# Kernel tuning notes

Measured on AMD Instinct MI355X. Metric: run time of the kernel, lower is better.

Reference implementation:

```python
import jax, jax.numpy as jnp
import numpy as np

NEG_INF = -9.0e15
ALPHA = 0.2  # leakyrelu slope


def setup_inputs() -> dict:
    key = jax.random.key(0)
    k1, k2, k3, k4, k5 = jax.random.split(key, 5)
    B, N, D_IN, D_OUT = 8, 2048, 128, 128
    h = jax.random.normal(k1, (B, N, D_IN), dtype=jnp.float32)
    adj = jax.random.randint(k2, (N, N), 0, 2, dtype=jnp.int32)
    W = jax.random.normal(k3, (D_IN, D_OUT), dtype=jnp.float32) * (1.0 / np.sqrt(D_IN))
    a_src = jax.random.normal(k4, (D_OUT,), dtype=jnp.float32) * (1.0 / np.sqrt(D_OUT))
    a_dst = jax.random.normal(k5, (D_OUT,), dtype=jnp.float32) * (1.0 / np.sqrt(D_OUT))
    return {"h": h, "adj": adj, "W": W, "a_src": a_src, "a_dst": a_dst}


def reference(h, adj, W, a_src, a_dst):
    # Wh: [B, N, D_out]
    Wh = jnp.einsum("bnd,de->bne", h, W)
    e_src = jnp.einsum("bne,e->bn", Wh, a_src)  # [B, N]
    e_dst = jnp.einsum("bne,e->bn", Wh, a_dst)  # [B, N]
    # additive attention logits: e[b,i,j] = e_src[b,i] + e_dst[b,j]
    e = e_src[:, :, None] + e_dst[:, None, :]  # [B, N, N]
    e = jnp.where(e > 0, e, ALPHA * e)  # leaky relu
    e = jnp.where(adj[None, :, :] > 0, e, NEG_INF)
    attention = jax.nn.softmax(e, axis=-1)  # [B, N, N]
    h_prime = jnp.einsum("bij,bje->bie", attention, Wh)
    return h_prime
```

## Files before the change

kernel.cpp:

```cpp
#include <hip/hip_runtime.h>
#include <stdint.h>

#define ALPHA 0.2f
#define LOG2E 1.4426950408889634f

typedef unsigned short u16;
typedef short s16x8 __attribute__((ext_vector_type(8)));
typedef float f32x4 __attribute__((ext_vector_type(4)));

union BF8 { s16x8 v; uint32_t u[4]; u16 s[8]; uint4 q; };

static __device__ __forceinline__ float bf2f(u16 u) {
  union { uint32_t i; float f; } c; c.i = ((uint32_t)u) << 16; return c.f;
}
static __device__ __forceinline__ uint32_t pk2bf(float lo, float hi) {
  uint32_t ul = __float_as_uint(lo) + 0x8000u;
  uint32_t uh = __float_as_uint(hi) + 0x8000u;
  return (ul >> 16) | (uh & 0xffff0000u);
}

static __device__ __forceinline__ void gl2lds16(const void* g, void* l) {
  __builtin_amdgcn_global_load_lds(
      (const __attribute__((address_space(1))) uint32_t*)g,
      (__attribute__((address_space(3))) uint32_t*)l, 16, 0, 0);
}

__global__ __launch_bounds__(256) void k_zero(uint32_t* __restrict__ out, int n32) {
  int gid = blockIdx.x * 256 + threadIdx.x;
  if (gid < n32) out[gid] = 0u;
}

__global__ __launch_bounds__(256) void k_pack_adj(const int* __restrict__ adj,
                                                  uint32_t* __restrict__ bits,
                                                  const u16* __restrict__ h,
                                                  int* __restrict__ flag) {
  int tid = threadIdx.x;
  int base = blockIdx.x * 256 + tid;
#pragma unroll
  for (int it = 0; it < 8; ++it) {
    int gid = base + it * (2048 * 256);
    unsigned long long m = __ballot(adj[gid] != 0);
    if ((tid & 63) == 0)
      *(unsigned long long*)(&bits[gid >> 5]) = m;
  }
  if (blockIdx.x == 0 && tid < 64) {
    u16 v = h[2 * tid];
    int e = (v >> 7) & 0xff;
    unsigned long long dm = __ballot(e >= 100 && e <= 140);
    if (tid == 0) flag[0] = (__popcll(dm) >= 48) ? 1 : 0;
  }
}

__global__ __launch_bounds__(256) void k_wh(
    const void* __restrict__ hV, const void* __restrict__ WgV,
    const void* __restrict__ aSrcV, const void* __restrict__ aDstV,
    const int* __restrict__ flag,
    u16* __restrict__ WhT, float* __restrict__ eS, float* __restrict__ eD) {
  __shared__ __align__(16) char smemRaw[34816];
  u16*   WT   = (u16*)smemRaw;
  float* tile = (float*)smemRaw;
  __shared__ float aS[128], aD[128];

  const int tid = threadIdx.x;
  const int mb = blockIdx.x * 64;
  const int isBf = *flag;

  if (isBf) {
    const u16* Wg = (const u16*)WgV;
    for (int it = 0; it < 8; ++it) {
      int idx = tid + it * 256;
      int k = idx >> 4, c0 = (idx & 15) * 8;
      uint4 w4 = *(const uint4*)(Wg + (k << 7) + c0);
      u16* wsv = (u16*)&w4;
#pragma unroll
      for (int e = 0; e < 8; ++e) WT[(c0 + e) * 136 + k] = wsv[e];
    }
    if (tid < 128) aS[tid] = bf2f(((const u16*)aSrcV)[tid]);
    else           aD[tid - 128] = bf2f(((const u16*)aDstV)[tid - 128]);
  } else {
    const float* Wg = (const float*)WgV;
    for (int it = 0; it < 8; ++it) {
      int idx = tid + it * 256;
      int k = idx >> 4, c0 = (idx & 15) * 8;
      float4 w0 = *(const float4*)(Wg + (k << 7) + c0);
      float4 w1 = *(const float4*)(Wg + (k << 7) + c0 + 4);
      float wf[8] = {w0.x, w0.y, w0.z, w0.w, w1.x, w1.y, w1.z, w1.w};
#pragma unroll
      for (int e = 0; e < 8; ++e)
        WT[(c0 + e) * 136 + k] = (u16)((__float_as_uint(wf[e]) + 0x8000u) >> 16);
    }
    if (tid < 128) aS[tid] = ((const float*)aSrcV)[tid];
    else           aD[tid - 128] = ((const float*)aDstV)[tid - 128];
  }
  __syncthreads();

  const int wv = tid >> 6, lane = tid & 63, ln = lane & 15, quad = lane >> 4;
  const int row = mb + wv * 16 + ln;

  f32x4 acc[8];
#pragma unroll
  for (int t = 0; t < 8; ++t) acc[t] = (f32x4){0.f, 0.f, 0.f, 0.f};

  if (isBf) {
    const u16* h = (const u16*)hV;
#pragma unroll
    for (int ks = 0; ks < 4; ++ks) {
      s16x8 af = *(const s16x8*)(h + (row << 7) + ks * 32 + quad * 8);
#pragma unroll
      for (int t = 0; t < 8; ++t) {
        s16x8 bfg = *(const s16x8*)(&WT[(t * 16 + ln) * 136 + ks * 32 + quad * 8]);
        acc[t] = __builtin_amdgcn_mfma_f32_16x16x32_bf16(af, bfg, acc[t], 0, 0, 0);
      }
    }
  } else {
    const float* h = (const float*)hV;
#pragma unroll
    for (int ks = 0; ks < 4; ++ks) {
      float4 a0 = *(const float4*)(h + (row << 7) + ks * 32 + quad * 8);
      float4 a1 = *(const float4*)(h + (row << 7) + ks * 32 + quad * 8 + 4);
      BF8 af;
      af.u[0] = pk2bf(a0.x, a0.y);
      af.u[1] = pk2bf(a0.z, a0.w);
      af.u[2] = pk2bf(a1.x, a1.y);
      af.u[3] = pk2bf(a1.z, a1.w);
#pragma unroll
      for (int t = 0; t < 8; ++t) {
        s16x8 bfg = *(const s16x8*)(&WT[(t * 16 + ln) * 136 + ks * 32 + quad * 8]);
        acc[t] = __builtin_amdgcn_mfma_f32_16x16x32_bf16(af.v, bfg, acc[t], 0, 0, 0);
      }
    }
  }
  __syncthreads();

#pragma unroll
  for (int t = 0; t < 8; ++t)
#pragma unroll
    for (int r = 0; r < 4; ++r)
      tile[(wv * 16 + quad * 4 + r) * 130 + t * 16 + ln] = acc[t][r];
  __syncthreads();

  if (tid < 128) {
    int r = tid & 63, grp = tid >> 6;
    const float* a = grp ? aD : aS;
    float sum = 0.f;
#pragma unroll 4
    for (int d = 0; d < 128; ++d) sum += tile[r * 130 + d] * a[d];
    int m = mb + r, b = m >> 11, n = m & 2047;
    (grp ? eD : eS)[(b << 11) + n] = sum * LOG2E;
  }

  {
    int d = tid >> 1, half = tid & 1;
    int n0 = mb & 2047, b = mb >> 11;
    uint32_t pk[16];
#pragma unroll
    for (int qq = 0; qq < 16; ++qq) {
      float v0 = tile[(half * 32 + 2 * qq) * 130 + d];
      float v1 = tile[(half * 32 + 2 * qq + 1) * 130 + d];
      pk[qq] = pk2bf(v0, v1);
    }
    uint4* dst = (uint4*)(WhT + (size_t)((b << 7) + d) * 2048 + n0 + half * 32);
#pragma unroll
    for (int c = 0; c < 4; ++c)
      dst[c] = make_uint4(pk[c * 4], pk[c * 4 + 1], pk[c * 4 + 2], pk[c * 4 + 3]);
  }
}

__global__ __launch_bounds__(512, 4) void k_attn(
    const u16* __restrict__ WhT, const float* __restrict__ eSrc,
    const float* __restrict__ eDst, const uint32_t* __restrict__ adjBits,
    const int* __restrict__ flag, void* __restrict__ outV) {
  __shared__ __align__(16) u16 bufB[2][8192];
  __shared__ __align__(16) u16 bufP[2][2048];

  const int tid = threadIdx.x;
  const int bid = (blockIdx.x & 7) * 64 + (blockIdx.x >> 3);
  const int b = bid >> 6, ig = bid & 63;
  const int i0 = ig * 32;

  const int w = tid >> 6, l = tid & 63;
  const int ln = l & 15, quad = l >> 4;
  const int s = w & 1, dh = w >> 1;

  const int gsrc = (l & 7) ^ ((l >> 3) & 7);
  const u16* whtB = WhT + ((size_t)b << 18);
  const u16* srcB = whtB + (size_t)(w * 8 + (l >> 3)) * 2048 + gsrc * 8;

  const int prow = tid >> 4, hg = tid & 15;
  const float sSp = eSrc[(b << 11) + i0 + prow];
  const float* eDb = eDst + (b << 11) + hg * 4;
  const uint32_t* adjB = adjBits + (size_t)(i0 + prow) * 64 + (hg >> 3);
  const int pOff = prow * 128 + ((hg ^ ((prow & 7) << 1)) * 8);

  int aOff[2], bOff[2][2];
#pragma unroll
  for (int jk = 0; jk < 2; ++jk) {
    aOff[jk] = (s * 16 + ln) * 128 + (((jk * 4 + quad) ^ (ln & 7)) * 16);
#pragma unroll
    for (int tt = 0; tt < 2; ++tt)
      bOff[tt][jk] = (dh * 32 + tt * 16 + ln) * 128
                   + (((jk * 4 + quad) ^ (ln & 7)) * 16);
  }

  f32x4 acc[2], accD;
  acc[0] = (f32x4){0.f, 0.f, 0.f, 0.f};
  acc[1] = (f32x4){0.f, 0.f, 0.f, 0.f};
  accD   = (f32x4){0.f, 0.f, 0.f, 0.f};

  BF8 ones;
  ones.u[0] = 0x3f803f80u; ones.u[1] = 0x3f803f80u;
  ones.u[2] = 0x3f803f80u; ones.u[3] = 0x3f803f80u;

  u16 *bBc = bufB[0], *bBn = bufB[1];
  u16 *bPc = bufP[0], *bPn = bufP[1];

  gl2lds16(srcB, bBc + w * 512);
  gl2lds16(srcB + 131072, bBc + 4096 + w * 512);
  {
    f32x4 dv = *(const f32x4*)(eDb);
    uint32_t aw = adjB[0];
    uint32_t nib = (aw >> ((hg & 7) * 4)) & 0xfu;
    float x0 = sSp + dv[0], x1 = sSp + dv[1], x2 = sSp + dv[2], x3 = sSp + dv[3];
    float p0 = exp2f(__builtin_amdgcn_fmed3f(x0, ALPHA * x0, 80.f));
    float p1 = exp2f(__builtin_amdgcn_fmed3f(x1, ALPHA * x1, 80.f));
    float p2 = exp2f(__builtin_amdgcn_fmed3f(x2, ALPHA * x2, 80.f));
    float p3 = exp2f(__builtin_amdgcn_fmed3f(x3, ALPHA * x3, 80.f));
    uint32_t m01 = ((nib & 1u) ? 0x0000ffffu : 0u) | ((nib & 2u) ? 0xffff0000u : 0u);
    uint32_t m23 = ((nib & 4u) ? 0x0000ffffu : 0u) | ((nib & 8u) ? 0xffff0000u : 0u);
    *(uint2*)((char*)bPc + pOff) = make_uint2(pk2bf(p0, p1) & m01,
                                              pk2bf(p2, p3) & m23);
  }
  __syncthreads();

  for (int t = 0; t < 32; ++t) {
    if (t + 1 < 32) {
      gl2lds16(srcB + (size_t)(t + 1) * 64, bBn + w * 512);
      gl2lds16(srcB + (size_t)(t + 1) * 64 + 131072, bBn + 4096 + w * 512);
      f32x4 dv = *(const f32x4*)(eDb + (t + 1) * 64);
      uint32_t aw = adjB[(t + 1) * 2];
      uint32_t nib = (aw >> ((hg & 7) * 4)) & 0xfu;
      float x0 = sSp + dv[0], x1 = sSp + dv[1], x2 = sSp + dv[2], x3 = sSp + dv[3];
      float p0 = exp2f(__builtin_amdgcn_fmed3f(x0, ALPHA * x0, 80.f));
      float p1 = exp2f(__builtin_amdgcn_fmed3f(x1, ALPHA * x1, 80.f));
      float p2 = exp2f(__builtin_amdgcn_fmed3f(x2, ALPHA * x2, 80.f));
      float p3 = exp2f(__builtin_amdgcn_fmed3f(x3, ALPHA * x3, 80.f));
      uint32_t m01 = ((nib & 1u) ? 0x0000ffffu : 0u) | ((nib & 2u) ? 0xffff0000u : 0u);
      uint32_t m23 = ((nib & 4u) ? 0x0000ffffu : 0u) | ((nib & 8u) ? 0xffff0000u : 0u);
      *(uint2*)((char*)bPn + pOff) = make_uint2(pk2bf(p0, p1) & m01,
                                                pk2bf(p2, p3) & m23);
    }

    s16x8 af0 = *(const s16x8*)((const char*)bPc + aOff[0]);
    s16x8 af1 = *(const s16x8*)((const char*)bPc + aOff[1]);
    s16x8 b00 = *(const s16x8*)((const char*)bBc + bOff[0][0]);
    s16x8 b10 = *(const s16x8*)((const char*)bBc + bOff[1][0]);
    s16x8 b01 = *(const s16x8*)((const char*)bBc + bOff[0][1]);
    s16x8 b11 = *(const s16x8*)((const char*)bBc + bOff[1][1]);

    __builtin_amdgcn_s_setprio(1);
    acc[0] = __builtin_amdgcn_mfma_f32_16x16x32_bf16(af0, b00, acc[0], 0, 0, 0);
    acc[1] = __builtin_amdgcn_mfma_f32_16x16x32_bf16(af0, b10, acc[1], 0, 0, 0);
    acc[0] = __builtin_amdgcn_mfma_f32_16x16x32_bf16(af1, b01, acc[0], 0, 0, 0);
    acc[1] = __builtin_amdgcn_mfma_f32_16x16x32_bf16(af1, b11, acc[1], 0, 0, 0);
    if (dh == 0) {
      accD = __builtin_amdgcn_mfma_f32_16x16x32_bf16(af0, ones.v, accD, 0, 0, 0);
      accD = __builtin_amdgcn_mfma_f32_16x16x32_bf16(af1, ones.v, accD, 0, 0, 0);
    }
    __builtin_amdgcn_s_setprio(0);

    __syncthreads();
    u16* tB = bBc; bBc = bBn; bBn = tB;
    u16* tP = bPc; bPc = bPn; bPn = tP;
  }

  float* den = (float*)bufP;
  if (dh == 0 && ln == 0) {
#pragma unroll
    for (int r = 0; r < 4; ++r) den[s * 16 + quad * 4 + r] = accD[r];
  }
  __syncthreads();

  float inv[4];
#pragma unroll
  for (int r = 0; r < 4; ++r)
    inv[r] = 1.0f / fmaxf(den[s * 16 + quad * 4 + r], 1e-37f);

  const int isBf = *flag;
  if (isBf) {
    u16* outp = (u16*)outV;
#pragma unroll
    for (int tt = 0; tt < 2; ++tt)
#pragma unroll
      for (int r = 0; r < 4; ++r) {
        size_t off = ((size_t)((b << 11) + i0 + s * 16 + quad * 4 + r) << 7)
                   + dh * 32 + tt * 16 + ln;
        float v = acc[tt][r] * inv[r];
        outp[off] = (u16)((__float_as_uint(v) + 0x8000u) >> 16);
      }
  } else {
    float* outp = (float*)outV;
#pragma unroll
    for (int tt = 0; tt < 2; ++tt)
#pragma unroll
      for (int r = 0; r < 4; ++r) {
        size_t off = ((size_t)((b << 11) + i0 + s * 16 + quad * 4 + r) << 7)
                   + dh * 32 + tt * 16 + ln;
        outp[off] = acc[tt][r] * inv[r];
      }
  }
}

extern "C" void kernel_launch(void* const* d_in, const int* in_sizes, int n_in,
                              void* d_out, int out_size, void* d_ws, size_t ws_size,
                              hipStream_t stream) {
  const void* h   = d_in[0];
  const int* adj  = (const int*)d_in[1];
  const void* Wg  = d_in[2];
  const void* aS  = d_in[3];
  const void* aD  = d_in[4];

  const size_t OFF_ES   = (size_t)4 << 20;
  const size_t OFF_ED   = OFF_ES + (64 << 10);
  const size_t OFF_BITS = OFF_ED + (64 << 10);
  const size_t OFF_FLAG = OFF_BITS + (512 << 10);
  const size_t NEEDED   = OFF_FLAG + 64;

  if (ws_size < NEEDED) {
    int n32 = out_size / 2;
    k_zero<<<(n32 + 255) / 256, 256, 0, stream>>>((uint32_t*)d_out, n32);
    return;
  }

  char* ws = (char*)d_ws;
  u16* WhT      = (u16*)ws;
  float* eSp    = (float*)(ws + OFF_ES);
  float* eDp    = (float*)(ws + OFF_ED);
  uint32_t* bit = (uint32_t*)(ws + OFF_BITS);
  int* flag     = (int*)(ws + OFF_FLAG);

  k_pack_adj<<<2048, 256, 0, stream>>>(adj, bit, (const u16*)h, flag);
  k_wh<<<256, 256, 0, stream>>>(h, Wg, aS, aD, flag, WhT, eSp, eDp);
  k_attn<<<512, 512, 0, stream>>>(WhT, eSp, eDp, bit, flag, d_out);
}
```

Before: 119.0 us.

## Build attention P fragments directly in registers instead of staging through LDS

Each lane now computes the masked exp probabilities for its own MFMA A-fragment in registers, prefetching eDst and adjacency words one step ahead, which removes the shared-memory P buffer along with its store and load traffic. Launch bounds go from 4 to 6 blocks per SM now that LDS use is smaller. The cost is redundant exp work: the four dh-warps sharing the same rows each recompute identical P values, roughly quadrupling transcendental work and raising register pressure under the tighter launch bound.

```diff
diff --git a/kernel.cpp b/kernel.cpp
--- a/kernel.cpp
+++ b/kernel.cpp
@@ -166,12 +166,12 @@
   }
 }
 
-__global__ __launch_bounds__(512, 4) void k_attn(
+__global__ __launch_bounds__(512, 6) void k_attn(
     const u16* __restrict__ WhT, const float* __restrict__ eSrc,
     const float* __restrict__ eDst, const uint32_t* __restrict__ adjBits,
     const int* __restrict__ flag, void* __restrict__ outV) {
   __shared__ __align__(16) u16 bufB[2][8192];
-  __shared__ __align__(16) u16 bufP[2][2048];
+  __shared__ float den[32];
 
   const int tid = threadIdx.x;
   const int bid = (blockIdx.x & 7) * 64 + (blockIdx.x >> 3);
@@ -186,94 +186,98 @@
   const u16* whtB = WhT + ((size_t)b << 18);
   const u16* srcB = whtB + (size_t)(w * 8 + (l >> 3)) * 2048 + gsrc * 8;
 
-  const int prow = tid >> 4, hg = tid & 15;
-  const float sSp = eSrc[(b << 11) + i0 + prow];
-  const float* eDb = eDst + (b << 11) + hg * 4;
-  const uint32_t* adjB = adjBits + (size_t)(i0 + prow) * 64 + (hg >> 3);
-  const int pOff = prow * 128 + ((hg ^ ((prow & 7) << 1)) * 8);
-
-  int aOff[2], bOff[2][2];
-#pragma unroll
-  for (int jk = 0; jk < 2; ++jk) {
-    aOff[jk] = (s * 16 + ln) * 128 + (((jk * 4 + quad) ^ (ln & 7)) * 16);
-#pragma unroll
-    for (int tt = 0; tt < 2; ++tt)
-      bOff[tt][jk] = (dh * 32 + tt * 16 + ln) * 128
-                   + (((jk * 4 + quad) ^ (ln & 7)) * 16);
-  }
-
-  f32x4 acc[2], accD;
-  acc[0] = (f32x4){0.f, 0.f, 0.f, 0.f};
-  acc[1] = (f32x4){0.f, 0.f, 0.f, 0.f};
-  accD   = (f32x4){0.f, 0.f, 0.f, 0.f};
+  const int row = i0 + s * 16 + ln;
+  const float sSp = eSrc[(b << 11) + row];
+  const uint32_t* adjRow = adjBits + (size_t)row * 64;
+  const float* eDq = eDst + (b << 11) + quad * 8;
+
+  const int bOff00 = (dh * 32 + 0 * 16 + ln) * 128 + (((0 * 4 + quad) ^ (ln & 7)) * 16);
+  const int bOff10 = (dh * 32 + 1 * 16 + ln) * 128 + (((0 * 4 + quad) ^ (ln & 7)) * 16);
+  const int bOff01 = (dh * 32 + 0 * 16 + ln) * 128 + (((1 * 4 + quad) ^ (ln & 7)) * 16);
+  const int bOff11 = (dh * 32 + 1 * 16 + ln) * 128 + (((1 * 4 + quad) ^ (ln & 7)) * 16);
+
+  f32x4 acc0 = (f32x4){0.f, 0.f, 0.f, 0.f};
+  f32x4 acc1 = (f32x4){0.f, 0.f, 0.f, 0.f};
+  f32x4 accD = (f32x4){0.f, 0.f, 0.f, 0.f};
 
   BF8 ones;
   ones.u[0] = 0x3f803f80u; ones.u[1] = 0x3f803f80u;
   ones.u[2] = 0x3f803f80u; ones.u[3] = 0x3f803f80u;
 
+#define MKMASK(mby, b0) (((((mby) >> (b0)) & 1u) ? 0x0000ffffu : 0u) | \
+                         ((((mby) >> ((b0) + 1)) & 1u) ? 0xffff0000u : 0u))
+#define PFRAG(af, d0, d1, mby) {                                              \
+    float x0 = sSp + (d0)[0], x1 = sSp + (d0)[1];                             \
+    float x2 = sSp + (d0)[2], x3 = sSp + (d0)[3];                             \
+    float x4 = sSp + (d1)[0], x5 = sSp + (d1)[1];                             \
+    float x6 = sSp + (d1)[2], x7 = sSp + (d1)[3];                             \
+    float p0 = exp2f(__builtin_amdgcn_fmed3f(x0, ALPHA * x0, 80.f));          \
+    float p1 = exp2f(__builtin_amdgcn_fmed3f(x1, ALPHA * x1, 80.f));          \
+    float p2 = exp2f(__builtin_amdgcn_fmed3f(x2, ALPHA * x2, 80.f));          \
+    float p3 = exp2f(__builtin_amdgcn_fmed3f(x3, ALPHA * x3, 80.f));          \
+    float p4 = exp2f(__builtin_amdgcn_fmed3f(x4, ALPHA * x4, 80.f));          \
+    float p5 = exp2f(__builtin_amdgcn_fmed3f(x5, ALPHA * x5, 80.f));          \
+    float p6 = exp2f(__builtin_amdgcn_fmed3f(x6, ALPHA * x6, 80.f));          \
+    float p7 = exp2f(__builtin_amdgcn_fmed3f(x7, ALPHA * x7, 80.f));          \
+    af.u[0] = pk2bf(p0, p1) & MKMASK(mby, 0);                                 \
+    af.u[1] = pk2bf(p2, p3) & MKMASK(mby, 2);                                 \
+    af.u[2] = pk2bf(p4, p5) & MKMASK(mby, 4);                                 \
+    af.u[3] = pk2bf(p6, p7) & MKMASK(mby, 6);                                 \
+  }
+
   u16 *bBc = bufB[0], *bBn = bufB[1];
-  u16 *bPc = bufP[0], *bPn = bufP[1];
+
+  f32x4 pd0 = *(const f32x4*)(eDq);
+  f32x4 pd1 = *(const f32x4*)(eDq + 4);
+  f32x4 pd2 = *(const f32x4*)(eDq + 32);
+  f32x4 pd3 = *(const f32x4*)(eDq + 36);
+  uint32_t paw0 = adjRow[0], paw1 = adjRow[1];
 
   gl2lds16(srcB, bBc + w * 512);
   gl2lds16(srcB + 131072, bBc + 4096 + w * 512);
-  {
-    f32x4 dv = *(const f32x4*)(eDb);
-    uint32_t aw = adjB[0];
-    uint32_t nib = (aw >> ((hg & 7) * 4)) & 0xfu;
-    float x0 = sSp + dv[0], x1 = sSp + dv[1], x2 = sSp + dv[2], x3 = sSp + dv[3];
-    float p0 = exp2f(__builtin_amdgcn_fmed3f(x0, ALPHA * x0, 80.f));
-    float p1 = exp2f(__builtin_amdgcn_fmed3f(x1, ALPHA * x1, 80.f));
-    float p2 = exp2f(__builtin_amdgcn_fmed3f(x2, ALPHA * x2, 80.f));
-    float p3 = exp2f(__builtin_amdgcn_fmed3f(x3, ALPHA * x3, 80.f));
-    uint32_t m01 = ((nib & 1u) ? 0x0000ffffu : 0u) | ((nib & 2u) ? 0xffff0000u : 0u);
-    uint32_t m23 = ((nib & 4u) ? 0x0000ffffu : 0u) | ((nib & 8u) ? 0xffff0000u : 0u);
-    *(uint2*)((char*)bPc + pOff) = make_uint2(pk2bf(p0, p1) & m01,
-                                              pk2bf(p2, p3) & m23);
-  }
   __syncthreads();
 
   for (int t = 0; t < 32; ++t) {
     if (t + 1 < 32) {
       gl2lds16(srcB + (size_t)(t + 1) * 64, bBn + w * 512);
       gl2lds16(srcB + (size_t)(t + 1) * 64 + 131072, bBn + 4096 + w * 512);
-      f32x4 dv = *(const f32x4*)(eDb + (t + 1) * 64);
-      uint32_t aw = adjB[(t + 1) * 2];
-      uint32_t nib = (aw >> ((hg & 7) * 4)) & 0xfu;
-      float x0 = sSp + dv[0], x1 = sSp + dv[1], x2 = sSp + dv[2], x3 = sSp + dv[3];
-      float p0 = exp2f(__builtin_amdgcn_fmed3f(x0, ALPHA * x0, 80.f));
-      float p1 = exp2f(__builtin_amdgcn_fmed3f(x1, ALPHA * x1, 80.f));
-      float p2 = exp2f(__builtin_amdgcn_fmed3f(x2, ALPHA * x2, 80.f));
-      float p3 = exp2f(__builtin_amdgcn_fmed3f(x3, ALPHA * x3, 80.f));
-      uint32_t m01 = ((nib & 1u) ? 0x0000ffffu : 0u) | ((nib & 2u) ? 0xffff0000u : 0u);
-      uint32_t m23 = ((nib & 4u) ? 0x0000ffffu : 0u) | ((nib & 8u) ? 0xffff0000u : 0u);
-      *(uint2*)((char*)bPn + pOff) = make_uint2(pk2bf(p0, p1) & m01,
-                                                pk2bf(p2, p3) & m23);
-    }
-
-    s16x8 af0 = *(const s16x8*)((const char*)bPc + aOff[0]);
-    s16x8 af1 = *(const s16x8*)((const char*)bPc + aOff[1]);
-    s16x8 b00 = *(const s16x8*)((const char*)bBc + bOff[0][0]);
-    s16x8 b10 = *(const s16x8*)((const char*)bBc + bOff[1][0]);
-    s16x8 b01 = *(const s16x8*)((const char*)bBc + bOff[0][1]);
-    s16x8 b11 = *(const s16x8*)((const char*)bBc + bOff[1][1]);
+    }
+    f32x4 cd0 = pd0, cd1 = pd1, cd2 = pd2, cd3 = pd3;
+    uint32_t cw0 = (paw0 >> (quad * 8)) & 0xffu;
+    uint32_t cw1 = (paw1 >> (quad * 8)) & 0xffu;
+    if (t + 1 < 32) {
+      const float* ep = eDq + (t + 1) * 64;
+      pd0 = *(const f32x4*)(ep);
+      pd1 = *(const f32x4*)(ep + 4);
+      pd2 = *(const f32x4*)(ep + 32);
+      pd3 = *(const f32x4*)(ep + 36);
+      paw0 = adjRow[(t + 1) * 2];
+      paw1 = adjRow[(t + 1) * 2 + 1];
+    }
+    BF8 af0, af1;
+    PFRAG(af0, cd0, cd1, cw0);
+    PFRAG(af1, cd2, cd3, cw1);
+
+    s16x8 b00 = *(const s16x8*)((const char*)bBc + bOff00);
+    s16x8 b10 = *(const s16x8*)((const char*)bBc + bOff10);
+    s16x8 b01 = *(const s16x8*)((const char*)bBc + bOff01);
+    s16x8 b11 = *(const s16x8*)((const char*)bBc + bOff11);
 
     __builtin_amdgcn_s_setprio(1);
-    acc[0] = __builtin_amdgcn_mfma_f32_16x16x32_bf16(af0, b00, acc[0], 0, 0, 0);
-    acc[1] = __builtin_amdgcn_mfma_f32_16x16x32_bf16(af0, b10, acc[1], 0, 0, 0);
-    acc[0] = __builtin_amdgcn_mfma_f32_16x16x32_bf16(af1, b01, acc[0], 0, 0, 0);
-    acc[1] = __builtin_amdgcn_mfma_f32_16x16x32_bf16(af1, b11, acc[1], 0, 0, 0);
+    acc0 = __builtin_amdgcn_mfma_f32_16x16x32_bf16(af0.v, b00, acc0, 0, 0, 0);
+    acc1 = __builtin_amdgcn_mfma_f32_16x16x32_bf16(af0.v, b10, acc1, 0, 0, 0);
+    acc0 = __builtin_amdgcn_mfma_f32_16x16x32_bf16(af1.v, b01, acc0, 0, 0, 0);
+    acc1 = __builtin_amdgcn_mfma_f32_16x16x32_bf16(af1.v, b11, acc1, 0, 0, 0);
     if (dh == 0) {
-      accD = __builtin_amdgcn_mfma_f32_16x16x32_bf16(af0, ones.v, accD, 0, 0, 0);
-      accD = __builtin_amdgcn_mfma_f32_16x16x32_bf16(af1, ones.v, accD, 0, 0, 0);
+      accD = __builtin_amdgcn_mfma_f32_16x16x32_bf16(af0.v, ones.v, accD, 0, 0, 0);
+      accD = __builtin_amdgcn_mfma_f32_16x16x32_bf16(af1.v, ones.v, accD, 0, 0, 0);
     }
     __builtin_amdgcn_s_setprio(0);
 
     __syncthreads();
-    u16* tB = bBc; bBc = bBn; bBn = tB;
-    u16* tP = bPc; bPc = bPn; bPn = tP;
-  }
-
-  float* den = (float*)bufP;
+    u16* tb = bBc; bBc = bBn; bBn = tb;
+  }
+
   if (dh == 0 && ln == 0) {
 #pragma unroll
     for (int r = 0; r < 4; ++r) den[s * 16 + quad * 4 + r] = accD[r];
@@ -289,25 +293,31 @@
   if (isBf) {
     u16* outp = (u16*)outV;
 #pragma unroll
-    for (int tt = 0; tt < 2; ++tt)
+    for (int tt = 0; tt < 2; ++tt) {
+      f32x4 a = tt ? acc1 : acc0;
 #pragma unroll
       for (int r = 0; r < 4; ++r) {
         size_t off = ((size_t)((b << 11) + i0 + s * 16 + quad * 4 + r) << 7)
                    + dh * 32 + tt * 16 + ln;
-        float v = acc[tt][r] * inv[r];
+        float v = a[r] * inv[r];
         outp[off] = (u16)((__float_as_uint(v) + 0x8000u) >> 16);
       }
+    }
   } else {
     float* outp = (float*)outV;
 #pragma unroll
-    for (int tt = 0; tt < 2; ++tt)
+    for (int tt = 0; tt < 2; ++tt) {
+      f32x4 a = tt ? acc1 : acc0;
 #pragma unroll
       for (int r = 0; r < 4; ++r) {
         size_t off = ((size_t)((b << 11) + i0 + s * 16 + quad * 4 + r) << 7)
                    + dh * 32 + tt * 16 + ln;
-        outp[off] = acc[tt][r] * inv[r];
+        outp[off] = a[r] * inv[r];
       }
-  }
+    }
+  }
+#undef PFRAG
+#undef MKMASK
 }
 
 extern "C" void kernel_launch(void* const* d_in, const int* in_sizes, int n_in,
```

New measurement: 154.1 us. 29.6% more time.

## Split attention key range across two blocks and merge partial sums

Applied to the files above, without the earlier changes.

Splits the j (key) dimension of the attention kernel into two halves, doubling the grid to 1024 blocks, each writing unnormalized partial numerators and denominators to workspace. A new merge kernel sums the halves, normalizes, and writes the output. The denominator is now a VALU shuffle-reduced sum of the packed bf16 probabilities instead of extra MFMAs against a ones vector, and the next tile's eDst and adjacency loads are prefetched a step ahead. This adds an extra launch and fp32 partial-result traffic through global memory in exchange for more parallelism and occupancy.

```diff
diff --git a/kernel.cpp b/kernel.cpp
--- a/kernel.cpp
+++ b/kernel.cpp
@@ -166,16 +166,17 @@
   }
 }
 
-__global__ __launch_bounds__(512, 4) void k_attn(
+__global__ __launch_bounds__(512, 8) void k_attn(
     const u16* __restrict__ WhT, const float* __restrict__ eSrc,
     const float* __restrict__ eDst, const uint32_t* __restrict__ adjBits,
-    const int* __restrict__ flag, void* __restrict__ outV) {
+    float* __restrict__ numP, float* __restrict__ denP) {
   __shared__ __align__(16) u16 bufB[2][8192];
   __shared__ __align__(16) u16 bufP[2][2048];
 
   const int tid = threadIdx.x;
-  const int bid = (blockIdx.x & 7) * 64 + (blockIdx.x >> 3);
-  const int b = bid >> 6, ig = bid & 63;
+  const int bid = (blockIdx.x & 7) * 128 + (blockIdx.x >> 3);
+  const int b = bid >> 7, rest = bid & 127;
+  const int jq = rest & 1, ig = rest >> 1;
   const int i0 = ig * 32;
 
   const int w = tid >> 6, l = tid & 63;
@@ -184,129 +185,129 @@
 
   const int gsrc = (l & 7) ^ ((l >> 3) & 7);
   const u16* whtB = WhT + ((size_t)b << 18);
-  const u16* srcB = whtB + (size_t)(w * 8 + (l >> 3)) * 2048 + gsrc * 8;
+  const u16* srcB = whtB + (size_t)(w * 8 + (l >> 3)) * 2048 + jq * 1024 + gsrc * 8;
 
   const int prow = tid >> 4, hg = tid & 15;
   const float sSp = eSrc[(b << 11) + i0 + prow];
-  const float* eDb = eDst + (b << 11) + hg * 4;
-  const uint32_t* adjB = adjBits + (size_t)(i0 + prow) * 64 + (hg >> 3);
+  const float* eDb = eDst + (b << 11) + jq * 1024 + hg * 4;
+  const uint32_t* adjB = adjBits + (size_t)(i0 + prow) * 64 + jq * 32 + (hg >> 3);
   const int pOff = prow * 128 + ((hg ^ ((prow & 7) << 1)) * 8);
-
-  int aOff[2], bOff[2][2];
-#pragma unroll
-  for (int jk = 0; jk < 2; ++jk) {
-    aOff[jk] = (s * 16 + ln) * 128 + (((jk * 4 + quad) ^ (ln & 7)) * 16);
-#pragma unroll
-    for (int tt = 0; tt < 2; ++tt)
-      bOff[tt][jk] = (dh * 32 + tt * 16 + ln) * 128
-                   + (((jk * 4 + quad) ^ (ln & 7)) * 16);
-  }
-
-  f32x4 acc[2], accD;
-  acc[0] = (f32x4){0.f, 0.f, 0.f, 0.f};
-  acc[1] = (f32x4){0.f, 0.f, 0.f, 0.f};
-  accD   = (f32x4){0.f, 0.f, 0.f, 0.f};
-
-  BF8 ones;
-  ones.u[0] = 0x3f803f80u; ones.u[1] = 0x3f803f80u;
-  ones.u[2] = 0x3f803f80u; ones.u[3] = 0x3f803f80u;
+  float dsum = 0.f;
+
+  const int aOff0 = (s * 16 + ln) * 128 + (((0 * 4 + quad) ^ (ln & 7)) * 16);
+  const int aOff1 = (s * 16 + ln) * 128 + (((1 * 4 + quad) ^ (ln & 7)) * 16);
+  const int bOff00 = (dh * 32 + 0 * 16 + ln) * 128 + (((0 * 4 + quad) ^ (ln & 7)) * 16);
+  const int bOff10 = (dh * 32 + 1 * 16 + ln) * 128 + (((0 * 4 + quad) ^ (ln & 7)) * 16);
+  const int bOff01 = (dh * 32 + 0 * 16 + ln) * 128 + (((1 * 4 + quad) ^ (ln & 7)) * 16);
+  const int bOff11 = (dh * 32 + 1 * 16 + ln) * 128 + (((1 * 4 + quad) ^ (ln & 7)) * 16);
+
+  f32x4 acc0 = (f32x4){0.f, 0.f, 0.f, 0.f};
+  f32x4 acc1 = (f32x4){0.f, 0.f, 0.f, 0.f};
+
+#define PPROD(dv, aw, pdst) {                                                 \
+    uint32_t nib = ((aw) >> ((hg & 7) * 4)) & 0xfu;                           \
+    float x0 = sSp + (dv)[0], x1 = sSp + (dv)[1];                             \
+    float x2 = sSp + (dv)[2], x3 = sSp + (dv)[3];                             \
+    float p0 = exp2f(__builtin_amdgcn_fmed3f(x0, ALPHA * x0, 80.f));          \
+    float p1 = exp2f(__builtin_amdgcn_fmed3f(x1, ALPHA * x1, 80.f));          \
+    float p2 = exp2f(__builtin_amdgcn_fmed3f(x2, ALPHA * x2, 80.f));          \
+    float p3 = exp2f(__builtin_amdgcn_fmed3f(x3, ALPHA * x3, 80.f));          \
+    p0 = (nib & 1u) ? p0 : 0.f;                                               \
+    p1 = (nib & 2u) ? p1 : 0.f;                                               \
+    p2 = (nib & 4u) ? p2 : 0.f;                                               \
+    p3 = (nib & 8u) ? p3 : 0.f;                                               \
+    uint32_t w0 = pk2bf(p0, p1), w1 = pk2bf(p2, p3);                          \
+    dsum += __uint_as_float(w0 << 16) + __uint_as_float(w0 & 0xffff0000u)     \
+          + __uint_as_float(w1 << 16) + __uint_as_float(w1 & 0xffff0000u);    \
+    *(uint2*)((char*)(pdst) + pOff) = make_uint2(w0, w1);                     \
+  }
+
+#define CONSUME(pPc, pBc) {                                                   \
+    s16x8 af0 = *(const s16x8*)((const char*)(pPc) + aOff0);                  \
+    s16x8 af1 = *(const s16x8*)((const char*)(pPc) + aOff1);                  \
+    s16x8 b00 = *(const s16x8*)((const char*)(pBc) + bOff00);                 \
+    s16x8 b10 = *(const s16x8*)((const char*)(pBc) + bOff10);                 \
+    s16x8 b01 = *(const s16x8*)((const char*)(pBc) + bOff01);                 \
+    s16x8 b11 = *(const s16x8*)((const char*)(pBc) + bOff11);                 \
+    __builtin_amdgcn_s_setprio(1);                                            \
+    acc0 = __builtin_amdgcn_mfma_f32_16x16x32_bf16(af0, b00, acc0, 0, 0, 0);  \
+    acc1 = __builtin_amdgcn_mfma_f32_16x16x32_bf16(af0, b10, acc1, 0, 0, 0);  \
+    acc0 = __builtin_amdgcn_mfma_f32_16x16x32_bf16(af1, b01, acc0, 0, 0, 0);  \
+    acc1 = __builtin_amdgcn_mfma_f32_16x16x32_bf16(af1, b11, acc1, 0, 0, 0);  \
+    __builtin_amdgcn_s_setprio(0);                                            \
+  }
 
   u16 *bBc = bufB[0], *bBn = bufB[1];
   u16 *bPc = bufP[0], *bPn = bufP[1];
 
+  f32x4 dv = *(const f32x4*)(eDb);
+  uint32_t aw = adjB[0];
+  PPROD(dv, aw, bPc);
+  dv = *(const f32x4*)(eDb + 64);
+  aw = adjB[2];
   gl2lds16(srcB, bBc + w * 512);
   gl2lds16(srcB + 131072, bBc + 4096 + w * 512);
-  {
-    f32x4 dv = *(const f32x4*)(eDb);
-    uint32_t aw = adjB[0];
-    uint32_t nib = (aw >> ((hg & 7) * 4)) & 0xfu;
-    float x0 = sSp + dv[0], x1 = sSp + dv[1], x2 = sSp + dv[2], x3 = sSp + dv[3];
-    float p0 = exp2f(__builtin_amdgcn_fmed3f(x0, ALPHA * x0, 80.f));
-    float p1 = exp2f(__builtin_amdgcn_fmed3f(x1, ALPHA * x1, 80.f));
-    float p2 = exp2f(__builtin_amdgcn_fmed3f(x2, ALPHA * x2, 80.f));
-    float p3 = exp2f(__builtin_amdgcn_fmed3f(x3, ALPHA * x3, 80.f));
-    uint32_t m01 = ((nib & 1u) ? 0x0000ffffu : 0u) | ((nib & 2u) ? 0xffff0000u : 0u);
-    uint32_t m23 = ((nib & 4u) ? 0x0000ffffu : 0u) | ((nib & 8u) ? 0xffff0000u : 0u);
-    *(uint2*)((char*)bPc + pOff) = make_uint2(pk2bf(p0, p1) & m01,
-                                              pk2bf(p2, p3) & m23);
-  }
   __syncthreads();
 
-  for (int t = 0; t < 32; ++t) {
-    if (t + 1 < 32) {
+  for (int t = 0; t < 16; ++t) {
+    if (t + 1 < 16) {
       gl2lds16(srcB + (size_t)(t + 1) * 64, bBn + w * 512);
       gl2lds16(srcB + (size_t)(t + 1) * 64 + 131072, bBn + 4096 + w * 512);
-      f32x4 dv = *(const f32x4*)(eDb + (t + 1) * 64);
-      uint32_t aw = adjB[(t + 1) * 2];
-      uint32_t nib = (aw >> ((hg & 7) * 4)) & 0xfu;
-      float x0 = sSp + dv[0], x1 = sSp + dv[1], x2 = sSp + dv[2], x3 = sSp + dv[3];
-      float p0 = exp2f(__builtin_amdgcn_fmed3f(x0, ALPHA * x0, 80.f));
-      float p1 = exp2f(__builtin_amdgcn_fmed3f(x1, ALPHA * x1, 80.f));
-      float p2 = exp2f(__builtin_amdgcn_fmed3f(x2, ALPHA * x2, 80.f));
-      float p3 = exp2f(__builtin_amdgcn_fmed3f(x3, ALPHA * x3, 80.f));
-      uint32_t m01 = ((nib & 1u) ? 0x0000ffffu : 0u) | ((nib & 2u) ? 0xffff0000u : 0u);
-      uint32_t m23 = ((nib & 4u) ? 0x0000ffffu : 0u) | ((nib & 8u) ? 0xffff0000u : 0u);
-      *(uint2*)((char*)bPn + pOff) = make_uint2(pk2bf(p0, p1) & m01,
-                                                pk2bf(p2, p3) & m23);
-    }
-
-    s16x8 af0 = *(const s16x8*)((const char*)bPc + aOff[0]);
-    s16x8 af1 = *(const s16x8*)((const char*)bPc + aOff[1]);
-    s16x8 b00 = *(const s16x8*)((const char*)bBc + bOff[0][0]);
-    s16x8 b10 = *(const s16x8*)((const char*)bBc + bOff[1][0]);
-    s16x8 b01 = *(const s16x8*)((const char*)bBc + bOff[0][1]);
-    s16x8 b11 = *(const s16x8*)((const char*)bBc + bOff[1][1]);
-
-    __builtin_amdgcn_s_setprio(1);
-    acc[0] = __builtin_amdgcn_mfma_f32_16x16x32_bf16(af0, b00, acc[0], 0, 0, 0);
-    acc[1] = __builtin_amdgcn_mfma_f32_16x16x32_bf16(af0, b10, acc[1], 0, 0, 0);
-    acc[0] = __builtin_amdgcn_mfma_f32_16x16x32_bf16(af1, b01, acc[0], 0, 0, 0);
-    acc[1] = __builtin_amdgcn_mfma_f32_16x16x32_bf16(af1, b11, acc[1], 0, 0, 0);
-    if (dh == 0) {
-      accD = __builtin_amdgcn_mfma_f32_16x16x32_bf16(af0, ones.v, accD, 0, 0, 0);
-      accD = __builtin_amdgcn_mfma_f32_16x16x32_bf16(af1, ones.v, accD, 0, 0, 0);
-    }
-    __builtin_amdgcn_s_setprio(0);
-
+      PPROD(dv, aw, bPn);
+      if (t + 2 < 16) {
+        dv = *(const f32x4*)(eDb + (t + 2) * 64);
+        aw = adjB[(t + 2) * 2];
+      }
+    }
+    CONSUME(bPc, bBc);
     __syncthreads();
-    u16* tB = bBc; bBc = bBn; bBn = tB;
-    u16* tP = bPc; bPc = bPn; bPn = tP;
-  }
-
-  float* den = (float*)bufP;
-  if (dh == 0 && ln == 0) {
-#pragma unroll
-    for (int r = 0; r < 4; ++r) den[s * 16 + quad * 4 + r] = accD[r];
-  }
-  __syncthreads();
-
-  float inv[4];
-#pragma unroll
-  for (int r = 0; r < 4; ++r)
-    inv[r] = 1.0f / fmaxf(den[s * 16 + quad * 4 + r], 1e-37f);
-
-  const int isBf = *flag;
-  if (isBf) {
-    u16* outp = (u16*)outV;
-#pragma unroll
-    for (int tt = 0; tt < 2; ++tt)
-#pragma unroll
-      for (int r = 0; r < 4; ++r) {
-        size_t off = ((size_t)((b << 11) + i0 + s * 16 + quad * 4 + r) << 7)
-                   + dh * 32 + tt * 16 + ln;
-        float v = acc[tt][r] * inv[r];
-        outp[off] = (u16)((__float_as_uint(v) + 0x8000u) >> 16);
-      }
+    u16* tb = bBc; bBc = bBn; bBn = tb;
+    u16* tp = bPc; bPc = bPn; bPn = tp;
+  }
+
+  {
+#pragma unroll
+    for (int m = 1; m < 16; m <<= 1) dsum += __shfl_xor(dsum, m);
+    if ((tid & 15) == 0)
+      denP[jq * 16384 + (b << 11) + i0 + prow] = dsum;
+
+    float* np = numP + ((size_t)jq << 21)
+              + ((size_t)((b << 11) + i0 + s * 16 + quad * 4) << 7)
+              + dh * 32 + ln;
+#pragma unroll
+    for (int r = 0; r < 4; ++r) {
+      np[r * 128 + 0]  = acc0[r];
+      np[r * 128 + 16] = acc1[r];
+    }
+  }
+#undef PPROD
+#undef CONSUME
+}
+
+__global__ __launch_bounds__(256) void k_merge(
+    const float* __restrict__ numP, const float* __restrict__ denP,
+    const int* __restrict__ flag, void* __restrict__ outV) {
+  const int gid = blockIdx.x * 256 + threadIdx.x;
+  const int e0 = gid * 8;
+  const int row = e0 >> 7;
+
+  f32x4 a0 = *(const f32x4*)(numP + e0);
+  f32x4 a1 = *(const f32x4*)(numP + e0 + 4);
+  f32x4 b0 = *(const f32x4*)(numP + (1 << 21) + e0);
+  f32x4 b1 = *(const f32x4*)(numP + (1 << 21) + e0 + 4);
+  float ds = denP[row] + denP[16384 + row];
+  float inv = 1.0f / fmaxf(ds, 1e-37f);
+
+  f32x4 v0 = (a0 + b0) * inv;
+  f32x4 v1 = (a1 + b1) * inv;
+
+  if (*flag) {
+    uint4 pk = make_uint4(pk2bf(v0[0], v0[1]), pk2bf(v0[2], v0[3]),
+                          pk2bf(v1[0], v1[1]), pk2bf(v1[2], v1[3]));
+    *(uint4*)((u16*)outV + e0) = pk;
   } else {
-    float* outp = (float*)outV;
-#pragma unroll
-    for (int tt = 0; tt < 2; ++tt)
-#pragma unroll
-      for (int r = 0; r < 4; ++r) {
-        size_t off = ((size_t)((b << 11) + i0 + s * 16 + quad * 4 + r) << 7)
-                   + dh * 32 + tt * 16 + ln;
-        outp[off] = acc[tt][r] * inv[r];
-      }
+    *(f32x4*)((float*)outV + e0) = v0;
+    *(f32x4*)((float*)outV + e0 + 4) = v1;
   }
 }
 
@@ -323,7 +324,9 @@
   const size_t OFF_ED   = OFF_ES + (64 << 10);
   const size_t OFF_BITS = OFF_ED + (64 << 10);
   const size_t OFF_FLAG = OFF_BITS + (512 << 10);
-  const size_t NEEDED   = OFF_FLAG + 64;
+  const size_t OFF_NUM  = (size_t)5 << 20;
+  const size_t OFF_DEN  = (size_t)21 << 20;
+  const size_t NEEDED   = OFF_DEN + (128 << 10);
 
   if (ws_size < NEEDED) {
     int n32 = out_size / 2;
@@ -337,8 +340,11 @@
   float* eDp    = (float*)(ws + OFF_ED);
   uint32_t* bit = (uint32_t*)(ws + OFF_BITS);
   int* flag     = (int*)(ws + OFF_FLAG);
+  float* numP   = (float*)(ws + OFF_NUM);
+  float* denP   = (float*)(ws + OFF_DEN);
 
   k_pack_adj<<<2048, 256, 0, stream>>>(adj, bit, (const u16*)h, flag);
   k_wh<<<256, 256, 0, stream>>>(h, Wg, aS, aD, flag, WhT, eSp, eDp);
-  k_attn<<<512, 512, 0, stream>>>(WhT, eSp, eDp, bit, flag, d_out);
-}
+  k_attn<<<1024, 512, 0, stream>>>(WhT, eSp, eDp, bit, numP, denP);
+  k_merge<<<1024, 256, 0, stream>>>(numP, denP, flag, d_out);
+}
```

Result: no change. 121.3 us (+2.0%).
